# Performance work log

Hardware: AMD Instinct MI355X
Metric: run time of the kernel (lower is better)

The kernel has to match this reference:

```python
import jax, jax.numpy as jnp
import numpy as np

N_LIG, N_PROT, K = 1024, 8192, 48
N = N_LIG + N_PROT
HID, FEAT, DEPTH = 256, 32, 5
NF = 6                      # sinusoid frequencies -> 12-dim distance embedding
EDGE_DIM = 4 * NF           # per-block dist emb (12) + top-level dist emb (12)
NORM = 5.0                  # agg_norm_factor
_FREQS = (2.0 * np.pi * 4.0 ** np.arange(NF) / 15.0).astype(np.float32)

def sin_emb(d2):
    # d2: [E,1] squared distances -> [E, 2*NF] sinusoidal embedding
    d = jnp.sqrt(d2 + 1e-8)
    x = d * _FREQS
    return jnp.concatenate([jnp.sin(x), jnp.cos(x)], axis=-1)

def knn_edges(coors):
    # KNN (k=48, no self loops) restricted to ligand query nodes (first N_LIG),
    # matching edges[:, :N_lig*k] slicing of knn_graph(flow='target_to_source').
    c = jax.lax.stop_gradient(coors)
    lig = c[:N_LIG]
    d2 = jnp.sum((lig[:, None, :] - c[None, :, :]) ** 2, axis=-1)  # [N_LIG, N]
    d2 = d2.at[jnp.arange(N_LIG), jnp.arange(N_LIG)].set(jnp.inf)
    _, idx = jax.lax.top_k(-d2, K)                                  # [N_LIG, K]
    row = jnp.repeat(jnp.arange(N_LIG), K)
    col = idx.reshape(-1)
    return row, col

def egnn(h, x, row, col, W_in, b_in, W_out, b_out, edge_W1, edge_b1, edge_W2, edge_b2, att_W, att_b, node_W1, node_b1, node_W2, node_b2, coord_W1, coord_b1, coord_W2, coord_b2, coord_W3):
    # EDM-style EGNN: per block 1 GCL (edge MLP + attention gate + node MLP residual)
    # followed by an equivariant coordinate update; sin distance embedding.
    emb0 = sin_emb(jnp.sum((x[row] - x[col]) ** 2, axis=-1, keepdims=True))
    h = h @ W_in + b_in
    for l in range(DEPTH):
        diff = x[row] - x[col]                         # [E,3]
        d2 = jnp.sum(diff ** 2, axis=-1, keepdims=True)
        cdiff = diff / (jnp.sqrt(d2 + 1e-8) + 1.0)     # norm_constant = 1
        ea = jnp.concatenate([sin_emb(d2), emb0], axis=-1)  # [E, EDGE_DIM]
        m = jax.nn.silu(jnp.concatenate([h[row], h[col], ea], axis=-1) @ edge_W1[l] + edge_b1[l])
        m = jax.nn.silu(m @ edge_W2[l] + edge_b2[l])
        m = m * jax.nn.sigmoid(m @ att_W[l] + att_b[l])         # attention gate
        agg = jax.ops.segment_sum(m, row, num_segments=N) / NORM
        u = jax.nn.silu(jnp.concatenate([h, agg], axis=-1) @ node_W1[l] + node_b1[l])
        h = h + (u @ node_W2[l] + node_b2[l])                    # residual node update
        c = jax.nn.silu(jnp.concatenate([h[row], h[col], ea], axis=-1) @ coord_W1[l] + coord_b1[l])  # use_latest_h
        c = jax.nn.silu(c @ coord_W2[l] + coord_b2[l])
        x = x + jax.ops.segment_sum(cdiff * (c @ coord_W3[l]), row, num_segments=N) / NORM
    return h @ W_out + b_out, x

def setup_inputs():
    key = jax.random.key(0)
    ks = jax.random.split(key, 24)
    f32 = jnp.float32
    def nrm(i, shape, scale=0.05):
        return jax.random.normal(ks[i], shape, dtype=f32) * scale
    return {
        'protein_positions': nrm(0, (N_PROT, 3), 3.0),
        'protein_ele': jax.random.randint(ks[1], (N_PROT,), 0, 5),
        'protein_amino_acid': jax.random.randint(ks[2], (N_PROT,), 0, 20),
        'protein_is_backbone': jax.random.randint(ks[3], (N_PROT,), 0, 2),
        'Xt_pos': nrm(4, (N_LIG, 3), 1.0),
        'Xt_features': nrm(5, (N_LIG, FEAT), 1.0),
        't': jax.random.randint(ks[6], (N_LIG,), 0, 1000),
        'Wt_time': nrm(7, (1000, 8), 1.0),
        'W_ele': nrm(8, (5, 16), 1.0),
        'W_aa': nrm(9, (20, 16), 1.0),
        'W_bb': nrm(10, (2, 8), 1.0),
        'W_in': nrm(11, (40, HID)), 'b_in': jnp.zeros((HID,), f32),
        'W_out': nrm(12, (HID, FEAT)), 'b_out': jnp.zeros((FEAT,), f32),
        'edge_W1': nrm(13, (DEPTH, 2 * HID + EDGE_DIM, HID)), 'edge_b1': jnp.zeros((DEPTH, HID), f32),
        'edge_W2': nrm(14, (DEPTH, HID, HID)), 'edge_b2': jnp.zeros((DEPTH, HID), f32),
        'att_W': nrm(15, (DEPTH, HID, 1)), 'att_b': jnp.zeros((DEPTH, 1), f32),
        'node_W1': nrm(16, (DEPTH, 2 * HID, HID)), 'node_b1': jnp.zeros((DEPTH, HID), f32),
        'node_W2': nrm(17, (DEPTH, HID, HID)), 'node_b2': jnp.zeros((DEPTH, HID), f32),
        'coord_W1': nrm(18, (DEPTH, 2 * HID + EDGE_DIM, HID)), 'coord_b1': jnp.zeros((DEPTH, HID), f32),
        'coord_W2': nrm(19, (DEPTH, HID, HID)), 'coord_b2': jnp.zeros((DEPTH, HID), f32),
        'coord_W3': nrm(20, (DEPTH, HID, 1), 0.001),
        'pos_w': jnp.ones((1, 1), f32),
    }

def reference(protein_positions, protein_ele, protein_amino_acid, protein_is_backbone, Xt_pos, Xt_features, t, Wt_time, W_ele, W_aa, W_bb, W_in, b_in, W_out, b_out, edge_W1, edge_b1, edge_W2, edge_b2, att_W, att_b, node_W1, node_b1, node_W2, node_b2, coord_W1, coord_b1, coord_W2, coord_b2, coord_W3, pos_w):
    prot_feat = jnp.concatenate([W_ele[protein_ele], W_aa[protein_amino_acid], W_bb[protein_is_backbone]], axis=-1)  # [N_PROT,40]
    feats = jnp.concatenate([jnp.concatenate([Xt_features, Wt_time[t]], axis=-1), prot_feat], axis=0)  # [N,40]
    coors = jnp.concatenate([Xt_pos, protein_positions], axis=0)  # [N,3]
    row, col = knn_edges(coors)
    h, x = egnn(feats, coors, row, col, W_in, b_in, W_out, b_out, edge_W1, edge_b1, edge_W2, edge_b2, att_W, att_b, node_W1, node_b1, node_W2, node_b2, coord_W1, coord_b1, coord_W2, coord_b2, coord_W3)
    # pos_linear: Linear(1,1,bias=False) applied elementwise == scalar multiply
    return x[:N_LIG] * pos_w[0, 0], h[:N_LIG]
```

## Files before the change

### kernel.cpp

```cpp
#include <hip/hip_runtime.h>
#include <hip/hip_bf16.h>
#include <math.h>

#define N_LIGC 1024
#define NTOT 9216
#define KNN 48
#define HID 256
#define DEPTHC 5
#define ETOT (N_LIGC*KNN)
#define KBINS 4096

typedef unsigned short u16;
typedef __attribute__((ext_vector_type(8))) short bf16x8;
typedef __attribute__((ext_vector_type(4))) float f32x4;

__device__ __forceinline__ float freq_f(int i){
  double p = (double)(1 << (2*i));
  return (float)((2.0*3.14159265358979323846)*p/15.0);
}
__device__ __forceinline__ float silu_f(float v){
  return v*__builtin_amdgcn_rcpf(1.0f+__expf(-v));
}
__device__ __forceinline__ float sigm_f(float v){
  return __builtin_amdgcn_rcpf(1.0f+__expf(-v));
}
// ... 19 lines not shown
  int Kt = Kp >> 5;
  int k0 = rest2 % Kt;
  int layer = rest2 / Kt;
  int kq = lane >> 4, nl = lane & 15;
  int kb = k0*32 + kq*8, n = n0*16 + nl;
  u16 o[8];
  #pragma unroll
  for (int j=0;j<8;j++){
    int k = kb + j;
    float v = (k < Keff) ? src[((size_t)layer*srcK + kOff + k)*N + n] : 0.f;
    o[j] = f2b_p(v);
  }
  *(uint4*)(dst + (size_t)idx*8) = *(uint4*)o;
}

__global__ __launch_bounds__(256) void k_packall(
    const float* eW1, const float* eW2, const float* nW1, const float* nW2,
    const float* cW1, const float* cW2, const float* Wout,
    u16* eW1abP, u16* eW1cP, u16* eW2p, u16* nW1p, u16* nW2p,
    u16* cW1abP, u16* cW1cP, u16* cW2p, u16* WoutP)
{
  int idx = blockIdx.x*256 + threadIdx.x;
  if (idx < 81920){ pack_one(eW1, eW1abP, 536, 0,   512, 512, 256, idx); return; } idx -= 81920;
  if (idx < 5120 ){ pack_one(eW1, eW1cP,  536, 512, 24,  32,  256, idx); return; } idx -= 5120;
  if (idx < 40960){ pack_one(eW2, eW2p,   256, 0,   256, 256, 256, idx); return; } idx -= 40960;
  if (idx < 81920){ pack_one(nW1, nW1p,   512, 0,   512, 512, 256, idx); return; } idx -= 81920;
  if (idx < 40960){ pack_one(nW2, nW2p,   256, 0,   256, 256, 256, idx); return; } idx -= 40960;
  if (idx < 81920){ pack_one(cW1, cW1abP, 536, 0,   512, 512, 256, idx); return; } idx -= 81920;
  if (idx < 5120 ){ pack_one(cW1, cW1cP,  536, 512, 24,  32,  256, idx); return; } idx -= 5120;
  if (idx < 40960){ pack_one(cW2, cW2p,   256, 0,   256, 256, 256, idx); return; } idx -= 40960;
  if (idx < 1024 ){ pack_one(Wout, WoutP, 256, 0,   256, 256, 32,  idx); return; }
}

__global__ __launch_bounds__(256) void k_embed_hinit(
    const float* __restrict__ protPos, const int* __restrict__ protEle,
    const int* __restrict__ protAA, const int* __restrict__ protBB,
    const float* __restrict__ XtPos, const float* __restrict__ XtFeat,
    const int* __restrict__ tArr, const float* __restrict__ WtTime,
    const float* __restrict__ Wele, const float* __restrict__ Waa,
    const float* __restrict__ Wbb,
    const float* __restrict__ Win, const float* __restrict__ bin,
    float* __restrict__ X0, float* __restrict__ X1,
    float* __restrict__ h, u16* __restrict__ h_bf)
{
  __shared__ float sF[8*40];
  int blk=blockIdx.x, tid=threadIdx.x;
  int n0=blk*8;
  for (int x=tid; x<344; x+=256){
    if (x < 320){
      int n = x/40, k = x%40;
      int node = n0+n;
      float v;
      if (node < N_LIGC){
        if (k < 32) v = XtFeat[node*32+k];
        else        v = WtTime[tArr[node]*8 + (k-32)];
      } else {
        int p = node - N_LIGC;
        if (k < 16)      v = Wele[protEle[p]*16 + k];
        else if (k < 32) v = Waa[protAA[p]*16 + (k-16)];
        else             v = Wbb[protBB[p]*8 + (k-32)];
      }
// ... 11 lines not shown
  #pragma unroll
  for (int n=0;n<8;n++) acc[n]=b;
  for (int k=0;k<40;k++){
    float w=Win[k*HID+tid];
    #pragma unroll
    for (int n=0;n<8;n++) acc[n]+=sF[n*40+k]*w;
  }
  #pragma unroll
  for (int n=0;n<8;n++){
    h[(size_t)(n0+n)*HID+tid]=acc[n];
    h_bf[(size_t)(n0+n)*HID+tid]=f2b_p(acc[n]);
  }
}

__global__ __launch_bounds__(256) void k_knn(const float* __restrict__ X,
    int* __restrict__ col, float* __restrict__ emb0)
{
  __shared__ unsigned int hist[KBINS];
  __shared__ unsigned int part[256];
  __shared__ float selD[KNN];
  __shared__ int   candI[512];
  __shared__ float candV[512];
  __shared__ int sB, sCless, sNeed, sNsel, sNcand;
  int b = blockIdx.x, tid = threadIdx.x;
  for (int i=tid;i<KBINS;i+=256) hist[i]=0u;
  if (tid==0){ sNsel=0; sNcand=0; }
  float px = X[b*3+0], py = X[b*3+1], pz = X[b*3+2];
  __syncthreads();
  #pragma unroll 4
  for (int j=0;j<36;j++){
    int i = tid + 256*j;
// ... 71 lines not shown
        int   os = __shfl_down(bslot, off);
        if (ov < bv || (ov==bv && oi<bi)){ bv=ov; bi=oi; bslot=os; }
      }
      int wslot = __shfl(bslot, 0);
      if (tid==0){ col[b*KNN+base+it]=bi; selD[base+it]=bv; }
      if ((wslot & 63) == tid) cv[wslot >> 6] = INFINITY;
    }
  }
  __syncthreads();
  if (tid < KNN){
    float d = sqrtf(selD[tid] + 1e-8f);
    int base = (b*KNN+tid)*12;
    #pragma unroll
    for (int i=0;i<6;i++){
      float fr = freq_f(i);
      emb0[base+i]   = sinf(d*fr);
      emb0[base+6+i] = cosf(d*fr);
    }
  }
}

__global__ __launch_bounds__(256) void k_pq(const u16* __restrict__ h_bf,
    const u16* __restrict__ Wab, float* __restrict__ R, u16* __restrict__ Qb, int l)
{
  __shared__ __align__(16) u16 sA[32*264];
  int blk=blockIdx.x, tid=threadIdx.x;
  int lane=tid&63, ng=tid>>6, quad=lane>>4, nl=lane&15;
  for (int t=tid; t<32*32; t+=256){
    int i=t>>5, q=t&31;
    uint4 v = ((const uint4*)(h_bf + (size_t)(blk*32+i)*HID))[q];
    *(uint4*)(sA + i*264 + q*8) = v;
  }
// ... 59 lines not shown
    #pragma unroll
    for (int nt=0;nt<4;nt++){
      int n = ng*64 + nt*16 + nl;
      #pragma unroll
      for (int r=0;r<4;r++){
        int node = blk*32 + mt*16 + quad*4 + r;
        R[(size_t)node*HID + n] = aR[mt][nt][r];
      }
    }
  }
}

__global__ __launch_bounds__(256,4) void k_comb_edge(
    const u16* __restrict__ Qb, const float* __restrict__ R,
    const float* __restrict__ xc,
    const int* __restrict__ colIdx, const float* __restrict__ emb0,
    const u16* __restrict__ W1cP, const float* __restrict__ B1,
    const u16* __restrict__ W2p, const float* __restrict__ B2,
    const float* __restrict__ attW, const float* __restrict__ attB,
    u16* __restrict__ agg_bf, int l)
{
  __shared__ __align__(16) u16 sQ[48*264];
  __shared__ __align__(16) u16 sEA[48*40];
  __shared__ float sR[256];
  __shared__ int sCol[48];
  __shared__ float sD[48];
  __shared__ float sSig[48];
  __shared__ float sDot[48][4];

  int row = blockIdx.x, tid = threadIdx.x;
  int lane = tid & 63, ng = tid >> 6;
// ... 2 lines not shown
  if (tid < 48) sCol[tid] = colIdx[(size_t)row*KNN + tid];
  sR[tid] = R[(size_t)row*HID + tid];
  __syncthreads();
  for (int t = tid; t < 48*32; t += 256){
    int e = t >> 5, q = t & 31;
    uint4 v = ((const uint4*)(Qb + (size_t)sCol[e]*HID))[q];
    *(uint4*)(sQ + e*264 + q*8) = v;
  }
  if (tid < 48){
    int cg = sCol[tid];
    float dx = xc[row*3+0]-xc[cg*3+0];
    float dy = xc[row*3+1]-xc[cg*3+1];
    float dz = xc[row*3+2]-xc[cg*3+2];
    float d = sqrtf(dx*dx+dy*dy+dz*dz + 1e-8f);
    sD[tid] = d;
    u16* ea = sEA + tid*40;
    #pragma unroll
    for (int i=0;i<12;i++) ea[12+i] = f2b_p(emb0[((size_t)row*KNN + tid)*12 + i]);
    #pragma unroll
    for (int i=24;i<32;i++) ea[i] = 0;
  }
  __syncthreads();
  for (int t=tid; t<288; t+=256){
    int e = t/6, i = t - 6*e;
    float fr = 0.41887903f * (float)(1 << (2*i));
    float x = sD[e]*fr;
    u16* ea = sEA + e*40;
    ea[i]   = f2b(__sinf(x));
    ea[6+i] = f2b(__cosf(x));
  }
  __syncthreads();

  f32x4 zero4 = {0.f,0.f,0.f,0.f};
// ... 113 lines not shown
    sgv[mt][r] = sSig[mt*16 + quad*4 + r];
  #pragma unroll
  for (int nt=0;nt<4;nt++){
    float a = 0.f;
    #pragma unroll
    for (int mt=0;mt<3;mt++)
    #pragma unroll
    for (int r=0;r<4;r++)
      a += acc2[mt][nt][r]*sgv[mt][r];
    a += __shfl_xor(a, 16);
    a += __shfl_xor(a, 32);
    if (quad == 0) agg_bf[(size_t)row*HID + ng*64 + nt*16 + nl] = f2b(a*0.2f);
  }
}

__global__ __launch_bounds__(256) void k_node(
    float* __restrict__ h, u16* __restrict__ h_bf,
    const u16* __restrict__ agg_bf,
    const u16* __restrict__ W1p, const float* __restrict__ B1,
    const u16* __restrict__ W2p, const float* __restrict__ B2,
    const u16* __restrict__ cWab, u16* __restrict__ QbC, float* __restrict__ RC,
    const u16* __restrict__ eWabN, u16* __restrict__ QbE, float* __restrict__ RE, int doE,
    const u16* __restrict__ WoutP, const float* __restrict__ bout,
    float* __restrict__ outH, int doOut, int l)
{
  __shared__ __align__(16) u16 sA[32*520];
  __shared__ __align__(16) u16 sU[32*264];
  u16* sH = sA;
  int blk=blockIdx.x, tid=threadIdx.x;
  int lane=tid&63, wv=tid>>6, quad=lane>>4, nl=lane&15;
  for (int t=tid; t<32*64; t+=256){
    int i=t>>6, q=t&63;
    int node = blk*32+i;
    uint4 v;
    if (q<32) v = ((const uint4*)(h_bf + (size_t)node*HID))[q];
    else if (node < N_LIGC) v = ((const uint4*)(agg_bf + (size_t)node*HID))[q-32];
    else { v.x=0u; v.y=0u; v.z=0u; v.w=0u; }
    *(uint4*)(sA + i*520 + q*8) = v;
  }
  __syncthreads();
  f32x4 zero4 = {0.f,0.f,0.f,0.f};
  f32x4 acc[2][4];
  #pragma unroll
  for (int i=0;i<2;i++){ acc[i][0]=zero4; acc[i][1]=zero4; acc[i][2]=zero4; acc[i][3]=zero4; }
  const u16* Wp = W1p + (size_t)l*512*HID;
  #pragma unroll 2
  for (int k0=0;k0<16;k0++){
    bf16x8 a0 = *(const bf16x8*)(sA + (0*16+nl)*520 + k0*32 + quad*8);
    bf16x8 a1 = *(const bf16x8*)(sA + (1*16+nl)*520 + k0*32 + quad*8);
    const u16* wb = Wp + ((size_t)(k0*16 + wv*4)*64 + lane)*8;
    bf16x8 b0 = *(const bf16x8*)(wb);
    bf16x8 b1 = *(const bf16x8*)(wb + 512);
    bf16x8 b2 = *(const bf16x8*)(wb + 1024);
    bf16x8 b3 = *(const bf16x8*)(wb + 1536);
    acc[0][0]=__builtin_amdgcn_mfma_f32_16x16x32_bf16(a0,b0,acc[0][0],0,0,0);
    acc[0][1]=__builtin_amdgcn_mfma_f32_16x16x32_bf16(a0,b1,acc[0][1],0,0,0);
    acc[0][2]=__builtin_amdgcn_mfma_f32_16x16x32_bf16(a0,b2,acc[0][2],0,0,0);
    acc[0][3]=__builtin_amdgcn_mfma_f32_16x16x32_bf16(a0,b3,acc[0][3],0,0,0);
    acc[1][0]=__builtin_amdgcn_mfma_f32_16x16x32_bf16(a1,b0,acc[1][0],0,0,0);
    acc[1][1]=__builtin_amdgcn_mfma_f32_16x16x32_bf16(a1,b1,acc[1][1],0,0,0);
    acc[1][2]=__builtin_amdgcn_mfma_f32_16x16x32_bf16(a1,b2,acc[1][2],0,0,0);
    acc[1][3]=__builtin_amdgcn_mfma_f32_16x16x32_bf16(a1,b3,acc[1][3],0,0,0);
  }
  #pragma unroll
  for (int mt=0;mt<2;mt++)
  #pragma unroll
  for (int nt=0;nt<4;nt++){
    int n = wv*64 + nt*16 + nl;
    float bb = B1[l*HID + n];
    #pragma unroll
    for (int r=0;r<4;r++){
      int m = mt*16 + quad*4 + r;
      sU[m*264 + n] = f2b(silu_f(acc[mt][nt][r] + bb));
    }
  }
  __syncthreads();
  f32x4 acc2[2][4];
  #pragma unroll
  for (int i=0;i<2;i++){ acc2[i][0]=zero4; acc2[i][1]=zero4; acc2[i][2]=zero4; acc2[i][3]=zero4; }
  const u16* W2 = W2p + (size_t)l*HID*HID;
  #pragma unroll 2
  for (int k0=0;k0<8;k0++){
    bf16x8 a0 = *(const bf16x8*)(sU + (0*16+nl)*264 + k0*32 + quad*8);
    bf16x8 a1 = *(const bf16x8*)(sU + (1*16+nl)*264 + k0*32 + quad*8);
    const u16* wb = W2 + ((size_t)(k0*16 + wv*4)*64 + lane)*8;
    bf16x8 b0 = *(const bf16x8*)(wb);
    bf16x8 b1 = *(const bf16x8*)(wb + 512);
    bf16x8 b2 = *(const bf16x8*)(wb + 1024);
    bf16x8 b3 = *(const bf16x8*)(wb + 1536);
    acc2[0][0]=__builtin_amdgcn_mfma_f32_16x16x32_bf16(a0,b0,acc2[0][0],0,0,0);
    acc2[0][1]=__builtin_amdgcn_mfma_f32_16x16x32_bf16(a0,b1,acc2[0][1],0,0,0);
    acc2[0][2]=__builtin_amdgcn_mfma_f32_16x16x32_bf16(a0,b2,acc2[0][2],0,0,0);
    acc2[0][3]=__builtin_amdgcn_mfma_f32_16x16x32_bf16(a0,b3,acc2[0][3],0,0,0);
    acc2[1][0]=__builtin_amdgcn_mfma_f32_16x16x32_bf16(a1,b0,acc2[1][0],0,0,0);
    acc2[1][1]=__builtin_amdgcn_mfma_f32_16x16x32_bf16(a1,b1,acc2[1][1],0,0,0);
    acc2[1][2]=__builtin_amdgcn_mfma_f32_16x16x32_bf16(a1,b2,acc2[1][2],0,0,0);
    acc2[1][3]=__builtin_amdgcn_mfma_f32_16x16x32_bf16(a1,b3,acc2[1][3],0,0,0);
  }
  #pragma unroll
  for (int mt=0;mt<2;mt++)
  #pragma unroll
  for (int nt=0;nt<4;nt++){
    int n = wv*64 + nt*16 + nl;
    float bb = B2[l*HID + n];
    #pragma unroll
    for (int r=0;r<4;r++){
      int m = mt*16 + quad*4 + r;
      size_t idx = (size_t)(blk*32+m)*HID + n;
      float v = h[idx] + acc2[mt][nt][r] + bb;
      h[idx] = v;
      u16 bv = f2b(v);
      h_bf[idx] = bv;
      sH[m*264 + n] = bv;
    }
  }
  __syncthreads();

  const u16* Wl = cWab + (size_t)l*512*HID;
  f32x4 q[2][4];
  #pragma unroll
  for (int i=0;i<2;i++){ q[i][0]=zero4; q[i][1]=zero4; q[i][2]=zero4; q[i][3]=zero4; }
  #pragma unroll 2
  for (int k0=0;k0<8;k0++){
    bf16x8 a0 = *(const bf16x8*)(sH + (0*16+nl)*264 + k0*32 + quad*8);
    bf16x8 a1 = *(const bf16x8*)(sH + (1*16+nl)*264 + k0*32 + quad*8);
    const u16* wb = Wl + ((size_t)((k0+8)*16 + wv*4)*64 + lane)*8;
    bf16x8 b0 = *(const bf16x8*)(wb);
    bf16x8 b1 = *(const bf16x8*)(wb + 512);
    bf16x8 b2 = *(const bf16x8*)(wb + 1024);
    bf16x8 b3 = *(const bf16x8*)(wb + 1536);
    q[0][0]=__builtin_amdgcn_mfma_f32_16x16x32_bf16(a0,b0,q[0][0],0,0,0);
    q[0][1]=__builtin_amdgcn_mfma_f32_16x16x32_bf16(a0,b1,q[0][1],0,0,0);
    q[0][2]=__builtin_amdgcn_mfma_f32_16x16x32_bf16(a0,b2,q[0][2],0,0,0);
    q[0][3]=__builtin_amdgcn_mfma_f32_16x16x32_bf16(a0,b3,q[0][3],0,0,0);
    q[1][0]=__builtin_amdgcn_mfma_f32_16x16x32_bf16(a1,b0,q[1][0],0,0,0);
    q[1][1]=__builtin_amdgcn_mfma_f32_16x16x32_bf16(a1,b1,q[1][1],0,0,0);
    q[1][2]=__builtin_amdgcn_mfma_f32_16x16x32_bf16(a1,b2,q[1][2],0,0,0);
    q[1][3]=__builtin_amdgcn_mfma_f32_16x16x32_bf16(a1,b3,q[1][3],0,0,0);
  }
  #pragma unroll
  for (int mt=0;mt<2;mt++)
  #pragma unroll
  for (int nt=0;nt<4;nt++){
    int n = wv*64 + nt*16 + nl;
    #pragma unroll
    for (int r=0;r<4;r++){
      int node = blk*32 + mt*16 + quad*4 + r;
      QbC[(size_t)node*HID + n] = f2b(q[mt][nt][r]);
    }
  }
  if (blk < 32){
    #pragma unroll
    for (int i=0;i<2;i++){ q[i][0]=zero4; q[i][1]=zero4; q[i][2]=zero4; q[i][3]=zero4; }
    #pragma unroll 2
    for (int k0=0;k0<8;k0++){
      bf16x8 a0 = *(const bf16x8*)(sH + (0*16+nl)*264 + k0*32 + quad*8);
      bf16x8 a1 = *(const bf16x8*)(sH + (1*16+nl)*264 + k0*32 + quad*8);
      const u16* wb = Wl + ((size_t)(k0*16 + wv*4)*64 + lane)*8;
      bf16x8 b0 = *(const bf16x8*)(wb);
      bf16x8 b1 = *(const bf16x8*)(wb + 512);
      bf16x8 b2 = *(const bf16x8*)(wb + 1024);
      bf16x8 b3 = *(const bf16x8*)(wb + 1536);
      q[0][0]=__builtin_amdgcn_mfma_f32_16x16x32_bf16(a0,b0,q[0][0],0,0,0);
      q[0][1]=__builtin_amdgcn_mfma_f32_16x16x32_bf16(a0,b1,q[0][1],0,0,0);
      q[0][2]=__builtin_amdgcn_mfma_f32_16x16x32_bf16(a0,b2,q[0][2],0,0,0);
      q[0][3]=__builtin_amdgcn_mfma_f32_16x16x32_bf16(a0,b3,q[0][3],0,0,0);
      q[1][0]=__builtin_amdgcn_mfma_f32_16x16x32_bf16(a1,b0,q[1][0],0,0,0);
      q[1][1]=__builtin_amdgcn_mfma_f32_16x16x32_bf16(a1,b1,q[1][1],0,0,0);
      q[1][2]=__builtin_amdgcn_mfma_f32_16x16x32_bf16(a1,b2,q[1][2],0,0,0);
      q[1][3]=__builtin_amdgcn_mfma_f32_16x16x32_bf16(a1,b3,q[1][3],0,0,0);
    }
    #pragma unroll
    for (int mt=0;mt<2;mt++)
    #pragma unroll
    for (int nt=0;nt<4;nt++){
      int n = wv*64 + nt*16 + nl;
      #pragma unroll
      for (int r=0;r<4;r++){
        int node = blk*32 + mt*16 + quad*4 + r;
        RC[(size_t)node*HID + n] = q[mt][nt][r];
      }
    }
  }
  if (doE){
    #pragma unroll
    for (int i=0;i<2;i++){ q[i][0]=zero4; q[i][1]=zero4; q[i][2]=zero4; q[i][3]=zero4; }
    #pragma unroll 2
    for (int k0=0;k0<8;k0++){
      bf16x8 a0 = *(const bf16x8*)(sH + (0*16+nl)*264 + k0*32 + quad*8);
      bf16x8 a1 = *(const bf16x8*)(sH + (1*16+nl)*264 + k0*32 + quad*8);
      const u16* wb = eWabN + ((size_t)((k0+8)*16 + wv*4)*64 + lane)*8;
      bf16x8 b0 = *(const bf16x8*)(wb);
      bf16x8 b1 = *(const bf16x8*)(wb + 512);
      bf16x8 b2 = *(const bf16x8*)(wb + 1024);
      bf16x8 b3 = *(const bf16x8*)(wb + 1536);
      q[0][0]=__builtin_amdgcn_mfma_f32_16x16x32_bf16(a0,b0,q[0][0],0,0,0);
      q[0][1]=__builtin_amdgcn_mfma_f32_16x16x32_bf16(a0,b1,q[0][1],0,0,0);
      q[0][2]=__builtin_amdgcn_mfma_f32_16x16x32_bf16(a0,b2,q[0][2],0,0,0);
      q[0][3]=__builtin_amdgcn_mfma_f32_16x16x32_bf16(a0,b3,q[0][3],0,0,0);
      q[1][0]=__builtin_amdgcn_mfma_f32_16x16x32_bf16(a1,b0,q[1][0],0,0,0);
      q[1][1]=__builtin_amdgcn_mfma_f32_16x16x32_bf16(a1,b1,q[1][1],0,0,0);
      q[1][2]=__builtin_amdgcn_mfma_f32_16x16x32_bf16(a1,b2,q[1][2],0,0,0);
      q[1][3]=__builtin_amdgcn_mfma_f32_16x16x32_bf16(a1,b3,q[1][3],0,0,0);
    }
    #pragma unroll
    for (int mt=0;mt<2;mt++)
    #pragma unroll
    for (int nt=0;nt<4;nt++){
      int n = wv*64 + nt*16 + nl;
      #pragma unroll
      for (int r=0;r<4;r++){
        int node = blk*32 + mt*16 + quad*4 + r;
        QbE[(size_t)node*HID + n] = f2b(q[mt][nt][r]);
      }
    }
    if (blk < 32){
      #pragma unroll
      for (int i=0;i<2;i++){ q[i][0]=zero4; q[i][1]=zero4; q[i][2]=zero4; q[i][3]=zero4; }
      #pragma unroll 2
      for (int k0=0;k0<8;k0++){
        bf16x8 a0 = *(const bf16x8*)(sH + (0*16+nl)*264 + k0*32 + quad*8);
        bf16x8 a1 = *(const bf16x8*)(sH + (1*16+nl)*264 + k0*32 + quad*8);
        const u16* wb = eWabN + ((size_t)(k0*16 + wv*4)*64 + lane)*8;
        bf16x8 b0 = *(const bf16x8*)(wb);
        bf16x8 b1 = *(const bf16x8*)(wb + 512);
        bf16x8 b2 = *(const bf16x8*)(wb + 1024);
        bf16x8 b3 = *(const bf16x8*)(wb + 1536);
        q[0][0]=__builtin_amdgcn_mfma_f32_16x16x32_bf16(a0,b0,q[0][0],0,0,0);
        q[0][1]=__builtin_amdgcn_mfma_f32_16x16x32_bf16(a0,b1,q[0][1],0,0,0);
        q[0][2]=__builtin_amdgcn_mfma_f32_16x16x32_bf16(a0,b2,q[0][2],0,0,0);
        q[0][3]=__builtin_amdgcn_mfma_f32_16x16x32_bf16(a0,b3,q[0][3],0,0,0);
        q[1][0]=__builtin_amdgcn_mfma_f32_16x16x32_bf16(a1,b0,q[1][0],0,0,0);
        q[1][1]=__builtin_amdgcn_mfma_f32_16x16x32_bf16(a1,b1,q[1][1],0,0,0);
        q[1][2]=__builtin_amdgcn_mfma_f32_16x16x32_bf16(a1,b2,q[1][2],0,0,0);
        q[1][3]=__builtin_amdgcn_mfma_f32_16x16x32_bf16(a1,b3,q[1][3],0,0,0);
      }
      #pragma unroll
      for (int mt=0;mt<2;mt++)
      #pragma unroll
      for (int nt=0;nt<4;nt++){
        int n = wv*64 + nt*16 + nl;
        #pragma unroll
        for (int r=0;r<4;r++){
          int node = blk*32 + mt*16 + quad*4 + r;
          RE[(size_t)node*HID + n] = q[mt][nt][r];
        }
      }
    }
  }
  if (doOut && blk < 32){
    int mt = wv >> 1, ntw = wv & 1;
    f32x4 o = zero4;
    #pragma unroll 2
    for (int k0=0;k0<8;k0++){
      bf16x8 a = *(const bf16x8*)(sH + (mt*16+nl)*264 + k0*32 + quad*8);
      bf16x8 b = *(const bf16x8*)(WoutP + ((size_t)(k0*2 + ntw)*64 + lane)*8);
      o = __builtin_amdgcn_mfma_f32_16x16x32_bf16(a,b,o,0,0,0);
    }
    int n = ntw*16 + nl;
    float bb = bout[n];
    #pragma unroll
    for (int r=0;r<4;r++){
      int m = mt*16 + quad*4 + r;
      outH[(size_t)(blk*32+m)*32 + n] = o[r] + bb;
    }
  }
}

__global__ __launch_bounds__(256,4) void k_comb_coord(
    const u16* __restrict__ Qb, const float* __restrict__ R,
    const float* __restrict__ xc, float* __restrict__ xn,
    const int* __restrict__ colIdx, const float* __restrict__ emb0,
    const u16* __restrict__ W1cP, const float* __restrict__ B1,
    const u16* __restrict__ W2p, const float* __restrict__ B2,
    const float* __restrict__ cW3,
    const float* __restrict__ posw, float* __restrict__ outX, int doOut, int l)
{
  __shared__ __align__(16) u16 sQ[48*264];
  __shared__ __align__(16) u16 sEA[48*40];
  __shared__ float sR[256];
  __shared__ int sCol[48];
  __shared__ float sD[48];
  __shared__ float sCd[48*3];
  __shared__ float sS[48];
  __shared__ float sDot[48][4];

  int row = blockIdx.x, tid = threadIdx.x;
// ... 5 lines not shown
  __syncthreads();
  for (int t = tid; t < 48*32; t += 256){
    int e = t >> 5, q = t & 31;
    uint4 v = ((const uint4*)(Qb + (size_t)sCol[e]*HID))[q];
    *(uint4*)(sQ + e*264 + q*8) = v;
  }
  if (tid < 48){
    int cg = sCol[tid];
    float dx = xc[row*3+0]-xc[cg*3+0];
    float dy = xc[row*3+1]-xc[cg*3+1];
    float dz = xc[row*3+2]-xc[cg*3+2];
    float d = sqrtf(dx*dx+dy*dy+dz*dz + 1e-8f);
    sD[tid] = d;
    float rden = __builtin_amdgcn_rcpf(d + 1.0f);
    sCd[tid*3+0]=dx*rden; sCd[tid*3+1]=dy*rden; sCd[tid*3+2]=dz*rden;
    u16* ea = sEA + tid*40;
    #pragma unroll
    for (int i=0;i<12;i++) ea[12+i] = f2b_p(emb0[((size_t)row*KNN + tid)*12 + i]);
    #pragma unroll
    for (int i=24;i<32;i++) ea[i] = 0;
  }
  __syncthreads();
  for (int t=tid; t<288; t+=256){
    int e = t/6, i = t - 6*e;
    float fr = 0.41887903f * (float)(1 << (2*i));
    float x = sD[e]*fr;
    u16* ea = sEA + e*40;
    ea[i]   = f2b(__sinf(x));
    ea[6+i] = f2b(__cosf(x));
  }
  __syncthreads();

  f32x4 zero4 = {0.f,0.f,0.f,0.f};
// ... 142 lines not shown
  const float* nW1     = (const float*)d_in[21];
  const float* nB1     = (const float*)d_in[22];
  const float* nW2     = (const float*)d_in[23];
  const float* nB2     = (const float*)d_in[24];
  const float* cW1     = (const float*)d_in[25];
  const float* cB1     = (const float*)d_in[26];
  const float* cW2     = (const float*)d_in[27];
  const float* cB2     = (const float*)d_in[28];
  const float* cW3     = (const float*)d_in[29];
  const float* posw    = (const float*)d_in[30];

  float* fp = (float*)d_ws;
  float* X0   = fp;               fp += NTOT*3;
  float* X1   = fp;               fp += NTOT*3;
  float* h    = fp;               fp += (size_t)NTOT*HID;
  float* emb0 = fp;               fp += (size_t)ETOT*12;
  float* RC   = fp;               fp += (size_t)N_LIGC*HID;
  float* RE   = fp;               fp += (size_t)N_LIGC*HID;
  int*   col  = (int*)fp;         fp += ETOT;
  u16*   up   = (u16*)fp;
  u16* h_bf   = up;               up += (size_t)NTOT*HID;
  u16* agg_bf = up;               up += (size_t)N_LIGC*HID;
  u16* QbE    = up;               up += (size_t)NTOT*HID;
  u16* QbC    = up;               up += (size_t)NTOT*HID;
  u16* eW1abP = up;               up += (size_t)DEPTHC*512*HID;
  u16* eW1cP  = up;               up += (size_t)DEPTHC*32*HID;
  u16* eW2p   = up;               up += (size_t)DEPTHC*HID*HID;
  u16* nW1p   = up;               up += (size_t)DEPTHC*512*HID;
  u16* nW2p   = up;               up += (size_t)DEPTHC*HID*HID;
  u16* cW1abP = up;               up += (size_t)DEPTHC*512*HID;
  u16* cW1cP  = up;               up += (size_t)DEPTHC*32*HID;
  u16* cW2p   = up;               up += (size_t)DEPTHC*HID*HID;
  u16* WoutP  = up;               up += (size_t)256*32;

  k_packall<<<1484,256,0,stream>>>(eW1,eW2,nW1,nW2,cW1,cW2,Wout,
      eW1abP,eW1cP,eW2p,nW1p,nW2p,cW1abP,cW1cP,cW2p,WoutP);
  k_embed_hinit<<<NTOT/8,256,0,stream>>>(protPos,protEle,protAA,protBB,XtPos,XtFeat,
      tArr,WtTime,Wele,Waa,Wbb,Win,bin,X0,X1,h,h_bf);
  k_knn<<<N_LIGC,256,0,stream>>>(X0,col,emb0);
  k_pq<<<NTOT/32,256,0,stream>>>(h_bf,eW1abP,RE,QbE,0);

  float* xc = X0; float* xn = X1;
  float* outF = (float*)d_out;
  for (int l=0;l<DEPTHC;l++){
    k_comb_edge<<<N_LIGC,256,0,stream>>>(QbE,RE,xc,col,emb0,eW1cP,eB1,eW2p,eB2,attW,attB,agg_bf,l);
    const u16* eNext = eW1abP + (size_t)((l+1)%DEPTHC)*512*HID;
    k_node<<<NTOT/32,256,0,stream>>>(h,h_bf,agg_bf,nW1p,nB1,nW2p,nB2,
        cW1abP,QbC,RC, eNext,QbE,RE,(l<DEPTHC-1)?1:0,
        WoutP,bout, outF+3072, (l==DEPTHC-1)?1:0, l);
    k_comb_coord<<<N_LIGC,256,0,stream>>>(QbC,RC,xc,xn,col,emb0,cW1cP,cB1,cW2p,cB2,cW3,
        posw, outF, (l==DEPTHC-1)?1:0, l);
    float* t2=xc; xc=xn; xn=t2;
  }
}
```

Baseline: 531.5 us.

## Retile node kernel to 36 rows per block, merge prep kernels, store emb0 as bf16

The node kernel now processes 36 nodes per block, padded to 48 rows, across exactly 256 blocks to match the device's CU count. This removes the partial second wave that 288 blocks of 32 caused, but about a quarter of the MFMA work is wasted on padding rows. The weight-packing and embedding/h-init kernels are merged into a single launch. emb0 is stored as bf16 so the edge and coord kernels read half the bytes and skip the per-element conversion.

```diff
diff --git a/kernel.cpp b/kernel.cpp
--- a/kernel.cpp
+++ b/kernel.cpp
@@ -9,6 +9,7 @@
 #define DEPTHC 5
 #define ETOT (N_LIGC*KNN)
 #define KBINS 4096
+#define PACK_BLKS 1484
 
 typedef unsigned short u16;
 typedef __attribute__((ext_vector_type(8))) short bf16x8;
@@ -58,25 +59,11 @@
   *(uint4*)(dst + (size_t)idx*8) = *(uint4*)o;
 }
 
-__global__ __launch_bounds__(256) void k_packall(
+__global__ __launch_bounds__(256) void k_prep(
     const float* eW1, const float* eW2, const float* nW1, const float* nW2,
     const float* cW1, const float* cW2, const float* Wout,
     u16* eW1abP, u16* eW1cP, u16* eW2p, u16* nW1p, u16* nW2p,
-    u16* cW1abP, u16* cW1cP, u16* cW2p, u16* WoutP)
-{
-  int idx = blockIdx.x*256 + threadIdx.x;
-  if (idx < 81920){ pack_one(eW1, eW1abP, 536, 0,   512, 512, 256, idx); return; } idx -= 81920;
-  if (idx < 5120 ){ pack_one(eW1, eW1cP,  536, 512, 24,  32,  256, idx); return; } idx -= 5120;
-  if (idx < 40960){ pack_one(eW2, eW2p,   256, 0,   256, 256, 256, idx); return; } idx -= 40960;
-  if (idx < 81920){ pack_one(nW1, nW1p,   512, 0,   512, 512, 256, idx); return; } idx -= 81920;
-  if (idx < 40960){ pack_one(nW2, nW2p,   256, 0,   256, 256, 256, idx); return; } idx -= 40960;
-  if (idx < 81920){ pack_one(cW1, cW1abP, 536, 0,   512, 512, 256, idx); return; } idx -= 81920;
-  if (idx < 5120 ){ pack_one(cW1, cW1cP,  536, 512, 24,  32,  256, idx); return; } idx -= 5120;
-  if (idx < 40960){ pack_one(cW2, cW2p,   256, 0,   256, 256, 256, idx); return; } idx -= 40960;
-  if (idx < 1024 ){ pack_one(Wout, WoutP, 256, 0,   256, 256, 32,  idx); return; }
-}
-
-__global__ __launch_bounds__(256) void k_embed_hinit(
+    u16* cW1abP, u16* cW1cP, u16* cW2p, u16* WoutP,
     const float* __restrict__ protPos, const int* __restrict__ protEle,
     const int* __restrict__ protAA, const int* __restrict__ protBB,
     const float* __restrict__ XtPos, const float* __restrict__ XtFeat,
@@ -88,7 +75,20 @@
     float* __restrict__ h, u16* __restrict__ h_bf)
 {
   __shared__ float sF[8*40];
-  int blk=blockIdx.x, tid=threadIdx.x;
+  if (blockIdx.x < PACK_BLKS){
+    int idx = blockIdx.x*256 + threadIdx.x;
+    if (idx < 81920){ pack_one(eW1, eW1abP, 536, 0,   512, 512, 256, idx); return; } idx -= 81920;
+    if (idx < 5120 ){ pack_one(eW1, eW1cP,  536, 512, 24,  32,  256, idx); return; } idx -= 5120;
+    if (idx < 40960){ pack_one(eW2, eW2p,   256, 0,   256, 256, 256, idx); return; } idx -= 40960;
+    if (idx < 81920){ pack_one(nW1, nW1p,   512, 0,   512, 512, 256, idx); return; } idx -= 81920;
+    if (idx < 40960){ pack_one(nW2, nW2p,   256, 0,   256, 256, 256, idx); return; } idx -= 40960;
+    if (idx < 81920){ pack_one(cW1, cW1abP, 536, 0,   512, 512, 256, idx); return; } idx -= 81920;
+    if (idx < 5120 ){ pack_one(cW1, cW1cP,  536, 512, 24,  32,  256, idx); return; } idx -= 5120;
+    if (idx < 40960){ pack_one(cW2, cW2p,   256, 0,   256, 256, 256, idx); return; } idx -= 40960;
+    if (idx < 1024 ){ pack_one(Wout, WoutP, 256, 0,   256, 256, 32,  idx); return; }
+    return;
+  }
+  int blk=blockIdx.x - PACK_BLKS, tid=threadIdx.x;
   int n0=blk*8;
   for (int x=tid; x<344; x+=256){
     if (x < 320){
@@ -130,7 +130,7 @@
 }
 
 __global__ __launch_bounds__(256) void k_knn(const float* __restrict__ X,
-    int* __restrict__ col, float* __restrict__ emb0)
+    int* __restrict__ col, u16* __restrict__ emb0)
 {
   __shared__ unsigned int hist[KBINS];
   __shared__ unsigned int part[256];
@@ -232,8 +232,8 @@
     #pragma unroll
     for (int i=0;i<6;i++){
       float fr = freq_f(i);
-      emb0[base+i]   = sinf(d*fr);
-      emb0[base+6+i] = cosf(d*fr);
+      emb0[base+i]   = f2b_p(sinf(d*fr));
+      emb0[base+6+i] = f2b_p(cosf(d*fr));
     }
   }
 }
@@ -323,7 +323,7 @@
 __global__ __launch_bounds__(256,4) void k_comb_edge(
     const u16* __restrict__ Qb, const float* __restrict__ R,
     const float* __restrict__ xc,
-    const int* __restrict__ colIdx, const float* __restrict__ emb0,
+    const int* __restrict__ colIdx, const u16* __restrict__ emb0,
     const u16* __restrict__ W1cP, const float* __restrict__ B1,
     const u16* __restrict__ W2p, const float* __restrict__ B2,
     const float* __restrict__ attW, const float* __restrict__ attB,
@@ -356,9 +356,11 @@
     float dz = xc[row*3+2]-xc[cg*3+2];
     float d = sqrtf(dx*dx+dy*dy+dz*dz + 1e-8f);
     sD[tid] = d;
+    const unsigned int* ep = (const unsigned int*)(emb0 + ((size_t)row*KNN + tid)*12);
+    unsigned int* dd = (unsigned int*)(sEA + tid*40 + 12);
+    #pragma unroll
+    for (int i=0;i<6;i++) dd[i] = ep[i];
     u16* ea = sEA + tid*40;
-    #pragma unroll
-    for (int i=0;i<12;i++) ea[12+i] = f2b_p(emb0[((size_t)row*KNN + tid)*12 + i]);
     #pragma unroll
     for (int i=24;i<32;i++) ea[i] = 0;
   }
@@ -502,7 +504,7 @@
   }
 }
 
-__global__ __launch_bounds__(256) void k_node(
+__global__ __launch_bounds__(256,1) void k_node(
     float* __restrict__ h, u16* __restrict__ h_bf,
     const u16* __restrict__ agg_bf,
     const u16* __restrict__ W1p, const float* __restrict__ B1,
@@ -512,30 +514,34 @@
     const u16* __restrict__ WoutP, const float* __restrict__ bout,
     float* __restrict__ outH, int doOut, int l)
 {
-  __shared__ __align__(16) u16 sA[32*520];
-  __shared__ __align__(16) u16 sU[32*264];
+  __shared__ __align__(16) u16 sA[48*520];
+  __shared__ __align__(16) u16 sU[48*264];
   u16* sH = sA;
   int blk=blockIdx.x, tid=threadIdx.x;
   int lane=tid&63, wv=tid>>6, quad=lane>>4, nl=lane&15;
-  for (int t=tid; t<32*64; t+=256){
+  int base = blk*36;
+  for (int t=tid; t<48*64; t+=256){
     int i=t>>6, q=t&63;
-    int node = blk*32+i;
     uint4 v;
-    if (q<32) v = ((const uint4*)(h_bf + (size_t)node*HID))[q];
-    else if (node < N_LIGC) v = ((const uint4*)(agg_bf + (size_t)node*HID))[q-32];
-    else { v.x=0u; v.y=0u; v.z=0u; v.w=0u; }
+    if (i < 36){
+      int node = base+i;
+      if (q<32) v = ((const uint4*)(h_bf + (size_t)node*HID))[q];
+      else if (node < N_LIGC) v = ((const uint4*)(agg_bf + (size_t)node*HID))[q-32];
+      else { v.x=0u; v.y=0u; v.z=0u; v.w=0u; }
+    } else { v.x=0u; v.y=0u; v.z=0u; v.w=0u; }
     *(uint4*)(sA + i*520 + q*8) = v;
   }
   __syncthreads();
   f32x4 zero4 = {0.f,0.f,0.f,0.f};
-  f32x4 acc[2][4];
-  #pragma unroll
-  for (int i=0;i<2;i++){ acc[i][0]=zero4; acc[i][1]=zero4; acc[i][2]=zero4; acc[i][3]=zero4; }
+  f32x4 acc[3][4];
+  #pragma unroll
+  for (int i=0;i<3;i++){ acc[i][0]=zero4; acc[i][1]=zero4; acc[i][2]=zero4; acc[i][3]=zero4; }
   const u16* Wp = W1p + (size_t)l*512*HID;
   #pragma unroll 2
   for (int k0=0;k0<16;k0++){
     bf16x8 a0 = *(const bf16x8*)(sA + (0*16+nl)*520 + k0*32 + quad*8);
     bf16x8 a1 = *(const bf16x8*)(sA + (1*16+nl)*520 + k0*32 + quad*8);
+    bf16x8 a2 = *(const bf16x8*)(sA + (2*16+nl)*520 + k0*32 + quad*8);
     const u16* wb = Wp + ((size_t)(k0*16 + wv*4)*64 + lane)*8;
     bf16x8 b0 = *(const bf16x8*)(wb);
     bf16x8 b1 = *(const bf16x8*)(wb + 512);
@@ -549,9 +555,13 @@
     acc[1][1]=__builtin_amdgcn_mfma_f32_16x16x32_bf16(a1,b1,acc[1][1],0,0,0);
     acc[1][2]=__builtin_amdgcn_mfma_f32_16x16x32_bf16(a1,b2,acc[1][2],0,0,0);
     acc[1][3]=__builtin_amdgcn_mfma_f32_16x16x32_bf16(a1,b3,acc[1][3],0,0,0);
-  }
-  #pragma unroll
-  for (int mt=0;mt<2;mt++)
+    acc[2][0]=__builtin_amdgcn_mfma_f32_16x16x32_bf16(a2,b0,acc[2][0],0,0,0);
+    acc[2][1]=__builtin_amdgcn_mfma_f32_16x16x32_bf16(a2,b1,acc[2][1],0,0,0);
+    acc[2][2]=__builtin_amdgcn_mfma_f32_16x16x32_bf16(a2,b2,acc[2][2],0,0,0);
+    acc[2][3]=__builtin_amdgcn_mfma_f32_16x16x32_bf16(a2,b3,acc[2][3],0,0,0);
+  }
+  #pragma unroll
+  for (int mt=0;mt<3;mt++)
   #pragma unroll
   for (int nt=0;nt<4;nt++){
     int n = wv*64 + nt*16 + nl;
@@ -563,14 +573,15 @@
     }
   }
   __syncthreads();
-  f32x4 acc2[2][4];
-  #pragma unroll
-  for (int i=0;i<2;i++){ acc2[i][0]=zero4; acc2[i][1]=zero4; acc2[i][2]=zero4; acc2[i][3]=zero4; }
+  f32x4 acc2[3][4];
+  #pragma unroll
+  for (int i=0;i<3;i++){ acc2[i][0]=zero4; acc2[i][1]=zero4; acc2[i][2]=zero4; acc2[i][3]=zero4; }
   const u16* W2 = W2p + (size_t)l*HID*HID;
   #pragma unroll 2
   for (int k0=0;k0<8;k0++){
     bf16x8 a0 = *(const bf16x8*)(sU + (0*16+nl)*264 + k0*32 + quad*8);
     bf16x8 a1 = *(const bf16x8*)(sU + (1*16+nl)*264 + k0*32 + quad*8);
+    bf16x8 a2 = *(const bf16x8*)(sU + (2*16+nl)*264 + k0*32 + quad*8);
     const u16* wb = W2 + ((size_t)(k0*16 + wv*4)*64 + lane)*8;
     bf16x8 b0 = *(const bf16x8*)(wb);
     bf16x8 b1 = *(const bf16x8*)(wb + 512);
@@ -584,9 +595,13 @@
     acc2[1][1]=__builtin_amdgcn_mfma_f32_16x16x32_bf16(a1,b1,acc2[1][1],0,0,0);
     acc2[1][2]=__builtin_amdgcn_mfma_f32_16x16x32_bf16(a1,b2,acc2[1][2],0,0,0);
     acc2[1][3]=__builtin_amdgcn_mfma_f32_16x16x32_bf16(a1,b3,acc2[1][3],0,0,0);
-  }
-  #pragma unroll
-  for (int mt=0;mt<2;mt++)
+    acc2[2][0]=__builtin_amdgcn_mfma_f32_16x16x32_bf16(a2,b0,acc2[2][0],0,0,0);
+    acc2[2][1]=__builtin_amdgcn_mfma_f32_16x16x32_bf16(a2,b1,acc2[2][1],0,0,0);
+    acc2[2][2]=__builtin_amdgcn_mfma_f32_16x16x32_bf16(a2,b2,acc2[2][2],0,0,0);
+    acc2[2][3]=__builtin_amdgcn_mfma_f32_16x16x32_bf16(a2,b3,acc2[2][3],0,0,0);
+  }
+  #pragma unroll
+  for (int mt=0;mt<3;mt++)
   #pragma unroll
   for (int nt=0;nt<4;nt++){
     int n = wv*64 + nt*16 + nl;
@@ -594,24 +609,30 @@
     #pragma unroll
     for (int r=0;r<4;r++){
       int m = mt*16 + quad*4 + r;
-      size_t idx = (size_t)(blk*32+m)*HID + n;
-      float v = h[idx] + acc2[mt][nt][r] + bb;
-      h[idx] = v;
-      u16 bv = f2b(v);
-      h_bf[idx] = bv;
-      sH[m*264 + n] = bv;
-    }
-  }
-  __syncthreads();
-
+      if (m < 36){
+        size_t idx = (size_t)(base+m)*HID + n;
+        float v = h[idx] + acc2[mt][nt][r] + bb;
+        h[idx] = v;
+        u16 bv = f2b(v);
+        h_bf[idx] = bv;
+        sH[m*264 + n] = bv;
+      } else {
+        sH[m*264 + n] = 0;
+      }
+    }
+  }
+  __syncthreads();
+
+  int isLig = (base < N_LIGC);
   const u16* Wl = cWab + (size_t)l*512*HID;
-  f32x4 q[2][4];
-  #pragma unroll
-  for (int i=0;i<2;i++){ q[i][0]=zero4; q[i][1]=zero4; q[i][2]=zero4; q[i][3]=zero4; }
+  f32x4 q[3][4];
+  #pragma unroll
+  for (int i=0;i<3;i++){ q[i][0]=zero4; q[i][1]=zero4; q[i][2]=zero4; q[i][3]=zero4; }
   #pragma unroll 2
   for (int k0=0;k0<8;k0++){
     bf16x8 a0 = *(const bf16x8*)(sH + (0*16+nl)*264 + k0*32 + quad*8);
     bf16x8 a1 = *(const bf16x8*)(sH + (1*16+nl)*264 + k0*32 + quad*8);
+    bf16x8 a2 = *(const bf16x8*)(sH + (2*16+nl)*264 + k0*32 + quad*8);
     const u16* wb = Wl + ((size_t)((k0+8)*16 + wv*4)*64 + lane)*8;
     bf16x8 b0 = *(const bf16x8*)(wb);
     bf16x8 b1 = *(const bf16x8*)(wb + 512);
@@ -625,25 +646,30 @@
     q[1][1]=__builtin_amdgcn_mfma_f32_16x16x32_bf16(a1,b1,q[1][1],0,0,0);
     q[1][2]=__builtin_amdgcn_mfma_f32_16x16x32_bf16(a1,b2,q[1][2],0,0,0);
     q[1][3]=__builtin_amdgcn_mfma_f32_16x16x32_bf16(a1,b3,q[1][3],0,0,0);
-  }
-  #pragma unroll
-  for (int mt=0;mt<2;mt++)
+    q[2][0]=__builtin_amdgcn_mfma_f32_16x16x32_bf16(a2,b0,q[2][0],0,0,0);
+    q[2][1]=__builtin_amdgcn_mfma_f32_16x16x32_bf16(a2,b1,q[2][1],0,0,0);
+    q[2][2]=__builtin_amdgcn_mfma_f32_16x16x32_bf16(a2,b2,q[2][2],0,0,0);
+    q[2][3]=__builtin_amdgcn_mfma_f32_16x16x32_bf16(a2,b3,q[2][3],0,0,0);
+  }
+  #pragma unroll
+  for (int mt=0;mt<3;mt++)
   #pragma unroll
   for (int nt=0;nt<4;nt++){
     int n = wv*64 + nt*16 + nl;
     #pragma unroll
     for (int r=0;r<4;r++){
-      int node = blk*32 + mt*16 + quad*4 + r;
-      QbC[(size_t)node*HID + n] = f2b(q[mt][nt][r]);
-    }
-  }
-  if (blk < 32){
-    #pragma unroll
-    for (int i=0;i<2;i++){ q[i][0]=zero4; q[i][1]=zero4; q[i][2]=zero4; q[i][3]=zero4; }
+      int m = mt*16 + quad*4 + r;
+      if (m < 36) QbC[(size_t)(base+m)*HID + n] = f2b(q[mt][nt][r]);
+    }
+  }
+  if (isLig){
+    #pragma unroll
+    for (int i=0;i<3;i++){ q[i][0]=zero4; q[i][1]=zero4; q[i][2]=zero4; q[i][3]=zero4; }
     #pragma unroll 2
     for (int k0=0;k0<8;k0++){
       bf16x8 a0 = *(const bf16x8*)(sH + (0*16+nl)*264 + k0*32 + quad*8);
       bf16x8 a1 = *(const bf16x8*)(sH + (1*16+nl)*264 + k0*32 + quad*8);
+      bf16x8 a2 = *(const bf16x8*)(sH + (2*16+nl)*264 + k0*32 + quad*8);
       const u16* wb = Wl + ((size_t)(k0*16 + wv*4)*64 + lane)*8;
       bf16x8 b0 = *(const bf16x8*)(wb);
       bf16x8 b1 = *(const bf16x8*)(wb + 512);
@@ -657,26 +683,32 @@
       q[1][1]=__builtin_amdgcn_mfma_f32_16x16x32_bf16(a1,b1,q[1][1],0,0,0);
       q[1][2]=__builtin_amdgcn_mfma_f32_16x16x32_bf16(a1,b2,q[1][2],0,0,0);
       q[1][3]=__builtin_amdgcn_mfma_f32_16x16x32_bf16(a1,b3,q[1][3],0,0,0);
-    }
-    #pragma unroll
-    for (int mt=0;mt<2;mt++)
+      q[2][0]=__builtin_amdgcn_mfma_f32_16x16x32_bf16(a2,b0,q[2][0],0,0,0);
+      q[2][1]=__builtin_amdgcn_mfma_f32_16x16x32_bf16(a2,b1,q[2][1],0,0,0);
+      q[2][2]=__builtin_amdgcn_mfma_f32_16x16x32_bf16(a2,b2,q[2][2],0,0,0);
+      q[2][3]=__builtin_amdgcn_mfma_f32_16x16x32_bf16(a2,b3,q[2][3],0,0,0);
+    }
+    #pragma unroll
+    for (int mt=0;mt<3;mt++)
     #pragma unroll
     for (int nt=0;nt<4;nt++){
       int n = wv*64 + nt*16 + nl;
       #pragma unroll
       for (int r=0;r<4;r++){
-        int node = blk*32 + mt*16 + quad*4 + r;
-        RC[(size_t)node*HID + n] = q[mt][nt][r];
+        int m = mt*16 + quad*4 + r;
+        int node = base + m;
+        if (m < 36 && node < N_LIGC) RC[(size_t)node*HID + n] = q[mt][nt][r];
       }
     }
   }
   if (doE){
     #pragma unroll
-    for (int i=0;i<2;i++){ q[i][0]=zero4; q[i][1]=zero4; q[i][2]=zero4; q[i][3]=zero4; }
+    for (int i=0;i<3;i++){ q[i][0]=zero4; q[i][1]=zero4; q[i][2]=zero4; q[i][3]=zero4; }
     #pragma unroll 2
     for (int k0=0;k0<8;k0++){
       bf16x8 a0 = *(const bf16x8*)(sH + (0*16+nl)*264 + k0*32 + quad*8);
       bf16x8 a1 = *(const bf16x8*)(sH + (1*16+nl)*264 + k0*32 + quad*8);
+      bf16x8 a2 = *(const bf16x8*)(sH + (2*16+nl)*264 + k0*32 + quad*8);
       const u16* wb = eWabN + ((size_t)((k0+8)*16 + wv*4)*64 + lane)*8;
       bf16x8 b0 = *(const bf16x8*)(wb);
       bf16x8 b1 = *(const bf16x8*)(wb + 512);
@@ -690,25 +722,30 @@
       q[1][1]=__builtin_amdgcn_mfma_f32_16x16x32_bf16(a1,b1,q[1][1],0,0,0);
       q[1][2]=__builtin_amdgcn_mfma_f32_16x16x32_bf16(a1,b2,q[1][2],0,0,0);
       q[1][3]=__builtin_amdgcn_mfma_f32_16x16x32_bf16(a1,b3,q[1][3],0,0,0);
-    }
-    #pragma unroll
-    for (int mt=0;mt<2;mt++)
+      q[2][0]=__builtin_amdgcn_mfma_f32_16x16x32_bf16(a2,b0,q[2][0],0,0,0);
+      q[2][1]=__builtin_amdgcn_mfma_f32_16x16x32_bf16(a2,b1,q[2][1],0,0,0);
+      q[2][2]=__builtin_amdgcn_mfma_f32_16x16x32_bf16(a2,b2,q[2][2],0,0,0);
+      q[2][3]=__builtin_amdgcn_mfma_f32_16x16x32_bf16(a2,b3,q[2][3],0,0,0);
+    }
+    #pragma unroll
+    for (int mt=0;mt<3;mt++)
     #pragma unroll
     for (int nt=0;nt<4;nt++){
       int n = wv*64 + nt*16 + nl;
       #pragma unroll
       for (int r=0;r<4;r++){
-        int node = blk*32 + mt*16 + quad*4 + r;
-        QbE[(size_t)node*HID + n] = f2b(q[mt][nt][r]);
-      }
-    }
-    if (blk < 32){
+        int m = mt*16 + quad*4 + r;
+        if (m < 36) QbE[(size_t)(base+m)*HID + n] = f2b(q[mt][nt][r]);
+      }
+    }
+    if (isLig){
       #pragma unroll
-      for (int i=0;i<2;i++){ q[i][0]=zero4; q[i][1]=zero4; q[i][2]=zero4; q[i][3]=zero4; }
+      for (int i=0;i<3;i++){ q[i][0]=zero4; q[i][1]=zero4; q[i][2]=zero4; q[i][3]=zero4; }
       #pragma unroll 2
       for (int k0=0;k0<8;k0++){
         bf16x8 a0 = *(const bf16x8*)(sH + (0*16+nl)*264 + k0*32 + quad*8);
         bf16x8 a1 = *(const bf16x8*)(sH + (1*16+nl)*264 + k0*32 + quad*8);
+        bf16x8 a2 = *(const bf16x8*)(sH + (2*16+nl)*264 + k0*32 + quad*8);
         const u16* wb = eWabN + ((size_t)(k0*16 + wv*4)*64 + lane)*8;
         bf16x8 b0 = *(const bf16x8*)(wb);
         bf16x8 b1 = *(const bf16x8*)(wb + 512);
@@ -722,35 +759,47 @@
         q[1][1]=__builtin_amdgcn_mfma_f32_16x16x32_bf16(a1,b1,q[1][1],0,0,0);
         q[1][2]=__builtin_amdgcn_mfma_f32_16x16x32_bf16(a1,b2,q[1][2],0,0,0);
         q[1][3]=__builtin_amdgcn_mfma_f32_16x16x32_bf16(a1,b3,q[1][3],0,0,0);
+        q[2][0]=__builtin_amdgcn_mfma_f32_16x16x32_bf16(a2,b0,q[2][0],0,0,0);
+        q[2][1]=__builtin_amdgcn_mfma_f32_16x16x32_bf16(a2,b1,q[2][1],0,0,0);
+        q[2][2]=__builtin_amdgcn_mfma_f32_16x16x32_bf16(a2,b2,q[2][2],0,0,0);
+        q[2][3]=__builtin_amdgcn_mfma_f32_16x16x32_bf16(a2,b3,q[2][3],0,0,0);
       }
       #pragma unroll
-      for (int mt=0;mt<2;mt++)
+      for (int mt=0;mt<3;mt++)
       #pragma unroll
       for (int nt=0;nt<4;nt++){
         int n = wv*64 + nt*16 + nl;
         #pragma unroll
         for (int r=0;r<4;r++){
-          int node = blk*32 + mt*16 + quad*4 + r;
-          RE[(size_t)node*HID + n] = q[mt][nt][r];
+          int m = mt*16 + quad*4 + r;
+          int node = base + m;
+          if (m < 36 && node < N_LIGC) RE[(size_t)node*HID + n] = q[mt][nt][r];
         }
       }
     }
   }
-  if (doOut && blk < 32){
-    int mt = wv >> 1, ntw = wv & 1;
-    f32x4 o = zero4;
+  if (doOut && isLig && wv < 2){
+    int ntw = wv;
+    f32x4 o[3]; o[0]=zero4; o[1]=zero4; o[2]=zero4;
     #pragma unroll 2
     for (int k0=0;k0<8;k0++){
-      bf16x8 a = *(const bf16x8*)(sH + (mt*16+nl)*264 + k0*32 + quad*8);
       bf16x8 b = *(const bf16x8*)(WoutP + ((size_t)(k0*2 + ntw)*64 + lane)*8);
-      o = __builtin_amdgcn_mfma_f32_16x16x32_bf16(a,b,o,0,0,0);
+      #pragma unroll
+      for (int mt=0;mt<3;mt++){
+        bf16x8 a = *(const bf16x8*)(sH + (mt*16+nl)*264 + k0*32 + quad*8);
+        o[mt] = __builtin_amdgcn_mfma_f32_16x16x32_bf16(a,b,o[mt],0,0,0);
+      }
     }
     int n = ntw*16 + nl;
     float bb = bout[n];
     #pragma unroll
+    for (int mt=0;mt<3;mt++)
+    #pragma unroll
     for (int r=0;r<4;r++){
       int m = mt*16 + quad*4 + r;
-      outH[(size_t)(blk*32+m)*32 + n] = o[r] + bb;
+      int node = base + m;
+      if (m < 36 && node < N_LIGC)
+        outH[(size_t)node*32 + n] = o[mt][r] + bb;
     }
   }
 }
@@ -758,7 +807,7 @@
 __global__ __launch_bounds__(256,4) void k_comb_coord(
     const u16* __restrict__ Qb, const float* __restrict__ R,
     const float* __restrict__ xc, float* __restrict__ xn,
-    const int* __restrict__ colIdx, const float* __restrict__ emb0,
+    const int* __restrict__ colIdx, const u16* __restrict__ emb0,
     const u16* __restrict__ W1cP, const float* __restrict__ B1,
     const u16* __restrict__ W2p, const float* __restrict__ B2,
     const float* __restrict__ cW3,
@@ -794,9 +843,11 @@
     sD[tid] = d;
     float rden = __builtin_amdgcn_rcpf(d + 1.0f);
     sCd[tid*3+0]=dx*rden; sCd[tid*3+1]=dy*rden; sCd[tid*3+2]=dz*rden;
+    const unsigned int* ep = (const unsigned int*)(emb0 + ((size_t)row*KNN + tid)*12);
+    unsigned int* dd = (unsigned int*)(sEA + tid*40 + 12);
+    #pragma unroll
+    for (int i=0;i<6;i++) dd[i] = ep[i];
     u16* ea = sEA + tid*40;
-    #pragma unroll
-    for (int i=0;i<12;i++) ea[12+i] = f2b_p(emb0[((size_t)row*KNN + tid)*12 + i]);
     #pragma unroll
     for (int i=24;i<32;i++) ea[i] = 0;
   }
@@ -969,11 +1020,11 @@
   float* X0   = fp;               fp += NTOT*3;
   float* X1   = fp;               fp += NTOT*3;
   float* h    = fp;               fp += (size_t)NTOT*HID;
-  float* emb0 = fp;               fp += (size_t)ETOT*12;
   float* RC   = fp;               fp += (size_t)N_LIGC*HID;
   float* RE   = fp;               fp += (size_t)N_LIGC*HID;
   int*   col  = (int*)fp;         fp += ETOT;
   u16*   up   = (u16*)fp;
+  u16* emb0   = up;               up += (size_t)ETOT*12;
   u16* h_bf   = up;               up += (size_t)NTOT*HID;
   u16* agg_bf = up;               up += (size_t)N_LIGC*HID;
   u16* QbE    = up;               up += (size_t)NTOT*HID;
@@ -988,9 +1039,9 @@
   u16* cW2p   = up;               up += (size_t)DEPTHC*HID*HID;
   u16* WoutP  = up;               up += (size_t)256*32;
 
-  k_packall<<<1484,256,0,stream>>>(eW1,eW2,nW1,nW2,cW1,cW2,Wout,
-      eW1abP,eW1cP,eW2p,nW1p,nW2p,cW1abP,cW1cP,cW2p,WoutP);
-  k_embed_hinit<<<NTOT/8,256,0,stream>>>(protPos,protEle,protAA,protBB,XtPos,XtFeat,
+  k_prep<<<PACK_BLKS + NTOT/8,256,0,stream>>>(eW1,eW2,nW1,nW2,cW1,cW2,Wout,
+      eW1abP,eW1cP,eW2p,nW1p,nW2p,cW1abP,cW1cP,cW2p,WoutP,
+      protPos,protEle,protAA,protBB,XtPos,XtFeat,
       tArr,WtTime,Wele,Waa,Wbb,Win,bin,X0,X1,h,h_bf);
   k_knn<<<N_LIGC,256,0,stream>>>(X0,col,emb0);
   k_pq<<<NTOT/32,256,0,stream>>>(h_bf,eW1abP,RE,QbE,0);
@@ -1000,7 +1051,7 @@
   for (int l=0;l<DEPTHC;l++){
     k_comb_edge<<<N_LIGC,256,0,stream>>>(QbE,RE,xc,col,emb0,eW1cP,eB1,eW2p,eB2,attW,attB,agg_bf,l);
     const u16* eNext = eW1abP + (size_t)((l+1)%DEPTHC)*512*HID;
-    k_node<<<NTOT/32,256,0,stream>>>(h,h_bf,agg_bf,nW1p,nB1,nW2p,nB2,
+    k_node<<<256,256,0,stream>>>(h,h_bf,agg_bf,nW1p,nB1,nW2p,nB2,
         cW1abP,QbC,RC, eNext,QbE,RE,(l<DEPTHC-1)?1:0,
         WoutP,bout, outF+3072, (l==DEPTHC-1)?1:0, l);
     k_comb_coord<<<N_LIGC,256,0,stream>>>(QbC,RC,xc,xn,col,emb0,cW1cP,cB1,cW2p,cB2,cW3,
```

New measurement: 549.7 us. 1.03x slower.
